# Kernel tuning notes

Hardware: AMD Instinct MI355X
Metric: run time of the kernel (lower is better)

Reference implementation:

```python
import jax, jax.numpy as jnp
import numpy as np

B, CIN, COUT, K, LDIM, HW = 16, 512, 512, 3, 512, 32


def setup_inputs() -> dict:
    key = jax.random.key(0)
    ks = jax.random.split(key, 4)
    return {
        "x": jax.random.normal(ks[0], (B, CIN, HW, HW), jnp.float32),
        "w": jax.random.normal(ks[1], (B, LDIM), jnp.float32),
        "mod_w": jax.random.normal(ks[2], (CIN, LDIM), jnp.float32) * 0.02,
        "mod_b": jnp.zeros((CIN,), jnp.float32),
        "ln_g": jnp.ones((CIN,), jnp.float32),
        "ln_b": jnp.zeros((CIN,), jnp.float32),
        "weight": jax.random.normal(ks[3], (COUT, CIN, K, K), jnp.float32) * 0.02,
        "scale": jnp.ones((1, CIN, 1, 1), jnp.float32),
    }


def reference(x, w, mod_w, mod_b, ln_g, ln_b, weight, scale):
    eps = 1e-8
    b, cin, H, W = x.shape
    cout, _, k, _ = weight.shape
    # modulation MLP: Linear -> LayerNorm -> LeakyReLU(0.2)
    s = w @ mod_w.T + mod_b                                   # [b, cin]
    mu = s.mean(-1, keepdims=True)
    var = s.var(-1, keepdims=True)
    s = (s - mu) * jax.lax.rsqrt(var + 1e-5) * ln_g + ln_b
    s = jnp.where(s >= 0, s, 0.2 * s)
    # modulate per-sample weights: [b, cout, cin, k, k]
    s = s.reshape(b, 1, cin, 1, 1) * scale.reshape(1, 1, cin, 1, 1)
    wmod = weight[None] * s
    # demodulate
    d = jax.lax.rsqrt(jnp.sum(wmod * wmod, axis=(2, 3, 4)) + eps)  # [b, cout]
    wmod = wmod * d.reshape(b, cout, 1, 1, 1)
    # batch-as-groups conv2d
    wg = wmod.reshape(b * cout, cin, k, k)
    xg = x.reshape(1, b * cin, H, W)
    pad = k // 2
    out = jax.lax.conv_general_dilated(
        xg, wg, window_strides=(1, 1), padding=[(pad, pad), (pad, pad)],
        dimension_numbers=("NCHW", "OIHW", "NCHW"), feature_group_count=b)
    return out.reshape(b, cout, H, W)
```

## Files before the change

### kernel.cpp

```cpp
#include <hip/hip_runtime.h>

typedef unsigned short u16;
typedef __bf16 bf16x8 __attribute__((ext_vector_type(8)));
typedef float  f32x16 __attribute__((ext_vector_type(16)));

__device__ __forceinline__ u16 f2bf(float f) {
    union { float f; unsigned u; } v; v.f = f;
    return (u16)((v.u + 0x7fffu + ((v.u >> 16) & 1u)) >> 16);
}

#define GLD16(gsrc, ldst) \
    __builtin_amdgcn_global_load_lds( \
        (const __attribute__((address_space(1))) void*)(gsrc), \
        (__attribute__((address_space(3))) void*)(ldst), 16, 0, 0)

__global__ __launch_bounds__(256) void lin_kernel(
    const float* __restrict__ w, const float* __restrict__ mod_w,
    const float* __restrict__ mod_b, float* __restrict__ s_raw)
{
    int gw = (blockIdx.x * 256 + threadIdx.x) >> 6;
    int lane = threadIdx.x & 63;
    int b = gw >> 9, c = gw & 511;
    const float* wr = w + b * 512;
    const float* mr = mod_w + (size_t)c * 512;
    float a = 0.f;
#pragma unroll
    for (int i = 0; i < 8; ++i)
        a = fmaf(wr[lane + i * 64], mr[lane + i * 64], a);
    for (int off = 32; off; off >>= 1) a += __shfl_down(a, off);
    if (!lane) s_raw[gw] = a + mod_b[c];
}

__global__ __launch_bounds__(512) void norm_kernel(
    const float* __restrict__ s_raw, const float* __restrict__ ln_g,
    const float* __restrict__ ln_b, const float* __restrict__ scale,
    float* __restrict__ s_eff)
{
    int b = blockIdx.x, c = threadIdx.x;
    __shared__ float rs[512], rq[512];
    float s = s_raw[b * 512 + c];
    rs[c] = s; rq[c] = s * s;
    __syncthreads();
    for (int off = 256; off; off >>= 1) {
        if (c < off) { rs[c] += rs[c + off]; rq[c] += rq[c + off]; }
        __syncthreads();
    }
    float mean = rs[0] * (1.f / 512.f);
    float var  = rq[0] * (1.f / 512.f) - mean * mean;
    float sn = (s - mean) * rsqrtf(var + 1e-5f) * ln_g[c] + ln_b[c];
    sn = sn >= 0.f ? sn : 0.2f * sn;
    s_eff[b * 512 + c] = sn * scale[c];
}

__global__ __launch_bounds__(256) void wsq_kernel(
    const float* __restrict__ weight, float* __restrict__ wsq, u16* __restrict__ wbfT)
{
    int idx = blockIdx.x * 256 + threadIdx.x;
    int co = idx >> 9, ci = idx & 511;
    int cg = ci >> 3, cj = ci & 7;
    const float* wp = weight + (size_t)idx * 9;
    float s = 0.f;
#pragma unroll
    for (int p = 0; p < 9; ++p) {
        float v = wp[p];
        s += v * v;
        wbfT[((size_t)(p * 64 + cg) * 512 + co) * 8 + cj] = f2bf(v);
    }
    wsq[idx] = s;
}

__global__ __launch_bounds__(256) void xs_kernel(
    const float* __restrict__ x, const float* __restrict__ s_eff,
    u16* __restrict__ xs)
{
    const int bh = blockIdx.x;
    const int b = bh >> 5, h = bh & 31;
    __shared__ float tile[64][33];
    for (int c0 = 0; c0 < 512; c0 += 64) {
        if (c0) __syncthreads();
        for (int idx = threadIdx.x; idx < 2048; idx += 256) {
            int c = idx >> 5, ww = idx & 31;
            tile[c][ww] = x[(((size_t)b * 512 + c0 + c) * 32 + h) * 32 + ww]
                          * s_eff[b * 512 + c0 + c];
        }
        __syncthreads();
        for (int idx = threadIdx.x; idx < 2048; idx += 256) {
            int ww = idx >> 6, c = idx & 63;
            xs[((b * 32 + h) * 32 + ww) * 512 + c0 + c] = f2bf(tile[c][ww]);
        }
    }
}

__global__ __launch_bounds__(256) void dsc_kernel(
    const float* __restrict__ s_eff, const float* __restrict__ wsq,
    float* __restrict__ dsc)
{
    int gw = (blockIdx.x * 256 + threadIdx.x) >> 6;
    int lane = threadIdx.x & 63;
    int b = gw >> 9, co = gw & 511;
    float a = 0.f;
#pragma unroll
    for (int i = 0; i < 8; ++i) {
        int cin = lane + i * 64;
        float se = s_eff[b * 512 + cin];
        a += se * se * wsq[co * 512 + cin];
    }
    for (int off = 32; off; off >>= 1) a += __shfl_down(a, off);
    if (!lane) dsc[gw] = rsqrtf(a + 1e-8f);
}

__global__ void zfill_kernel(float* p) { p[threadIdx.x] = 0.f; }

__global__ __launch_bounds__(512) void conv_kernel(
    const u16* __restrict__ wbfT,
    const u16* __restrict__ xs,
    const float* __restrict__ dsc,
    const u16* __restrict__ zp,
    float* __restrict__ out)
{
    __shared__ __align__(16) u16 ldsA[2][24576];
    __shared__ __align__(16) u16 ldsB[2][8192];

    const int tid  = threadIdx.x;
    const int lane = tid & 63;
    const int wv   = tid >> 6;
    const int wm   = wv >> 1;
    const int wn   = wv & 1;
    const int l31  = lane & 31;
    const int kc8  = lane >> 5;

    const int bx = blockIdx.x;
    const int mt = bx & 1;
    const int nt = bx >> 1;
    const int b  = nt >> 3;
    const int h0 = (nt & 7) << 2;

    const u16* xsb = xs + (size_t)b * (32 * 32 * 512);

    const u16* asrc[6];
#pragma unroll
    for (int k = 0; k < 6; ++k) {
        int ch = tid + k * 512;
        int pp = ch >> 10, kc = (ch >> 8) & 3, co = ch & 255;
        asrc[k] = wbfT + ((size_t)(pp * 64 + kc) * 512 + mt * 256 + co) * 8;
    }
    auto stageA = [&](int buf) {
        char* d = (char*)ldsA[buf] + wv * 1024;
#pragma unroll
        for (int k = 0; k < 6; ++k) GLD16(asrc[k], d + k * 8192);
    };
    auto advA = [&](int dkf) {
#pragma unroll
        for (int k = 0; k < 6; ++k) asrc[k] += (long)dkf * 4096;
    };

    const u16* bsrc[2]; bool binb[2];
#pragma unroll
    for (int k = 0; k < 2; ++k) {
        int ch = tid + k * 512;
        int kc = ch / 204, p = ch % 204;
        int rr = p / 34, cc = p % 34;
        int hh = h0 - 1 + rr, ww = cc - 1;
        binb[k] = (ch < 816) && ((unsigned)hh < 32u) && ((unsigned)ww < 32u);
        bsrc[k] = xsb + (hh * 32 + ww) * 512 + kc * 8;
    }
    auto stageB = [&](int buf) {
        char* d = (char*)ldsB[buf] + wv * 1024;
        GLD16(binb[0] ? bsrc[0] : zp, d);
        GLD16(binb[1] ? bsrc[1] : zp, d + 8192);
    };

    f32x16 acc[2][2] = {};

    stageA(0);
    advA(192);
    stageB(0);
    __syncthreads();

    int pidx = 0;
    for (int r = 0; r < 16; ++r) {
        const char* Bb = (const char*)ldsB[r & 1];
        const bool lastR = (r == 15);

#pragma unroll
        for (int phi = 0; phi < 3; ++phi) {
            const int abuf = pidx & 1;
            const char* Ab = (const char*)ldsA[abuf];
            const bool lastPhase = lastR && (phi == 2);

            if (!lastPhase) {
                stageA(abuf ^ 1);
                advA(phi == 1 ? -380 : 192);
            }
            if (phi == 1 && !lastR) {
#pragma unroll
                for (int k = 0; k < 2; ++k) bsrc[k] += 32;
                stageB((r + 1) & 1);
            }

            bf16x8 af[3][2][2], bfr[3][2][2];
#pragma unroll
            for (int pp = 0; pp < 3; ++pp)
#pragma unroll
                for (int kk = 0; kk < 2; ++kk) {
                    const int kc = kk * 2 + kc8;
#pragma unroll
                    for (int mf = 0; mf < 2; ++mf) {
                        int co = wm * 64 + mf * 32 + l31;
                        af[pp][mf][kk] = *reinterpret_cast<const bf16x8*>(
                            Ab + (((pp * 4 + kc) * 256 + co) << 4));
                    }
#pragma unroll
                    for (int nf = 0; nf < 2; ++nf) {
                        int p = (wn * 2 + nf + phi) * 34 + l31 + pp;
                        bfr[pp][nf][kk] = *reinterpret_cast<const bf16x8*>(
                            Bb + ((kc * 204 + p) << 4));
                    }
                }

#pragma unroll
            for (int pp = 0; pp < 3; ++pp)
#pragma unroll
                for (int kk = 0; kk < 2; ++kk) {
                    acc[0][0] = __builtin_amdgcn_mfma_f32_32x32x16_bf16(
                        af[pp][0][kk], bfr[pp][0][kk], acc[0][0], 0, 0, 0);
                    acc[0][1] = __builtin_amdgcn_mfma_f32_32x32x16_bf16(
                        af[pp][0][kk], bfr[pp][1][kk], acc[0][1], 0, 0, 0);
                    acc[1][0] = __builtin_amdgcn_mfma_f32_32x32x16_bf16(
                        af[pp][1][kk], bfr[pp][0][kk], acc[1][0], 0, 0, 0);
                    acc[1][1] = __builtin_amdgcn_mfma_f32_32x32x16_bf16(
                        af[pp][1][kk], bfr[pp][1][kk], acc[1][1], 0, 0, 0);
                }

            if (!lastPhase) __syncthreads();
            ++pidx;
        }
    }

    const float* db = dsc + b * 512;
#pragma unroll
    for (int mf = 0; mf < 2; ++mf) {
#pragma unroll
        for (int nf = 0; nf < 2; ++nf) {
            const int h = h0 + wn * 2 + nf, w = l31;
#pragma unroll
            for (int q = 0; q < 16; ++q) {
                int row = (q & 3) + 8 * (q >> 2) + 4 * kc8;
                int co  = mt * 256 + wm * 64 + mf * 32 + row;
                out[(((size_t)b * 512 + co) * 32 + h) * 32 + w]
                    = acc[mf][nf][q] * db[co];
            }
        }
    }
}

extern "C" void kernel_launch(void* const* d_in, const int* in_sizes, int n_in,
                              void* d_out, int out_size, void* d_ws, size_t ws_size,
                              hipStream_t stream) {
    const float* x      = (const float*)d_in[0];
    const float* w      = (const float*)d_in[1];
    const float* mod_w  = (const float*)d_in[2];
    const float* mod_b  = (const float*)d_in[3];
    const float* ln_g   = (const float*)d_in[4];
    const float* ln_b   = (const float*)d_in[5];
    const float* weight = (const float*)d_in[6];
    const float* scale  = (const float*)d_in[7];
    float* out = (float*)d_out;

    char* ws = (char*)d_ws;
    float* s_raw = (float*)(ws);
    float* dsc   = (float*)(ws);
    float* s_eff = (float*)(ws + 32768);
    float* wsq   = (float*)(ws + 65536);
    u16*   wbfT  = (u16*)(ws + 65536 + 1048576);
    u16*   xs    = (u16*)(ws + 65536 + 1048576 + 4718592);
    if (ws_size < 22609920u) return;

    lin_kernel <<<2048, 256, 0, stream>>>(w, mod_w, mod_b, s_raw);
    wsq_kernel <<<1024, 256, 0, stream>>>(weight, wsq, wbfT);
    norm_kernel<<<16, 512, 0, stream>>>(s_raw, ln_g, ln_b, scale, s_eff);
    xs_kernel  <<<512, 256, 0, stream>>>(x, s_eff, xs);
    dsc_kernel <<<2048, 256, 0, stream>>>(s_eff, wsq, dsc);
    zfill_kernel<<<1, 1024, 0, stream>>>(s_eff);
    conv_kernel<<<256, 512, 0, stream>>>(wbfT, xs, dsc, (const u16*)s_eff, out);
}
```

Before: 121.4 us.

## Load weight fragments directly from global into registers, drop LDS A staging

The conv kernel no longer stages the modulated weight tiles through shared memory. Each wave reads its A fragments straight from global memory into registers, double-buffered one phase ahead. The input tile is now staged through registers and ordinary LDS stores, and only one barrier per row iteration remains instead of one per phase. This removes the large A LDS buffer and most barriers, but adds register pressure and duplicate global reads of weights across waves that share the same rows.

```diff
diff --git a/kernel.cpp b/kernel.cpp
--- a/kernel.cpp
+++ b/kernel.cpp
@@ -8,11 +8,6 @@
     union { float f; unsigned u; } v; v.f = f;
     return (u16)((v.u + 0x7fffu + ((v.u >> 16) & 1u)) >> 16);
 }
-
-#define GLD16(gsrc, ldst) \
-    __builtin_amdgcn_global_load_lds( \
-        (const __attribute__((address_space(1))) void*)(gsrc), \
-        (__attribute__((address_space(3))) void*)(ldst), 16, 0, 0)
 
 __global__ __launch_bounds__(256) void lin_kernel(
     const float* __restrict__ w, const float* __restrict__ mod_w,
@@ -118,7 +113,6 @@
     const u16* __restrict__ zp,
     float* __restrict__ out)
 {
-    __shared__ __align__(16) u16 ldsA[2][24576];
     __shared__ __align__(16) u16 ldsB[2][8192];
 
     const int tid  = threadIdx.x;
@@ -137,24 +131,10 @@
 
     const u16* xsb = xs + (size_t)b * (32 * 32 * 512);
 
-    const u16* asrc[6];
-#pragma unroll
-    for (int k = 0; k < 6; ++k) {
-        int ch = tid + k * 512;
-        int pp = ch >> 10, kc = (ch >> 8) & 3, co = ch & 255;
-        asrc[k] = wbfT + ((size_t)(pp * 64 + kc) * 512 + mt * 256 + co) * 8;
-    }
-    auto stageA = [&](int buf) {
-        char* d = (char*)ldsA[buf] + wv * 1024;
-#pragma unroll
-        for (int k = 0; k < 6; ++k) GLD16(asrc[k], d + k * 8192);
-    };
-    auto advA = [&](int dkf) {
-#pragma unroll
-        for (int k = 0; k < 6; ++k) asrc[k] += (long)dkf * 4096;
-    };
-
-    const u16* bsrc[2]; bool binb[2];
+    const u16* abase = wbfT + ((size_t)(mt * 256 + wm * 64 + l31)) * 8
+                            + (size_t)kc8 * 4096;
+
+    const u16* bptr[2]; bool binb[2]; int bdst[2];
 #pragma unroll
     for (int k = 0; k < 2; ++k) {
         int ch = tid + k * 512;
@@ -162,78 +142,89 @@
         int rr = p / 34, cc = p % 34;
         int hh = h0 - 1 + rr, ww = cc - 1;
         binb[k] = (ch < 816) && ((unsigned)hh < 32u) && ((unsigned)ww < 32u);
-        bsrc[k] = xsb + (hh * 32 + ww) * 512 + kc * 8;
-    }
-    auto stageB = [&](int buf) {
-        char* d = (char*)ldsB[buf] + wv * 1024;
-        GLD16(binb[0] ? bsrc[0] : zp, d);
-        GLD16(binb[1] ? bsrc[1] : zp, d + 8192);
-    };
+        bptr[k] = binb[k] ? xsb + (hh * 32 + ww) * 512 + kc * 8 : zp;
+        bdst[k] = ch * 16;
+    }
+    const int badv[2] = { binb[0] ? 32 : 0, binb[1] ? 32 : 0 };
 
     f32x16 acc[2][2] = {};
-
-    stageA(0);
-    advA(192);
-    stageB(0);
-    __syncthreads();
-
-    int pidx = 0;
+    bf16x8 af[2][3][2][2];
+    uint4  bst[2];
+
+#pragma unroll
+    for (int k = 0; k < 2; ++k) {
+        bst[k] = *reinterpret_cast<const uint4*>(bptr[k]);
+        bptr[k] += badv[k];
+        *reinterpret_cast<uint4*>((char*)ldsB[0] + bdst[k]) = bst[k];
+    }
+#pragma unroll
+    for (int pp = 0; pp < 3; ++pp)
+#pragma unroll
+        for (int mf = 0; mf < 2; ++mf)
+#pragma unroll
+            for (int kk = 0; kk < 2; ++kk)
+                af[0][pp][mf][kk] = *reinterpret_cast<const bf16x8*>(
+                    abase + (size_t)(pp * 64 + 2 * kk) * 4096 + mf * 256);
+    asm volatile("s_waitcnt lgkmcnt(0)" ::: "memory");
+    __builtin_amdgcn_s_barrier();
+
+#pragma unroll
     for (int r = 0; r < 16; ++r) {
-        const char* Bb = (const char*)ldsB[r & 1];
-        const bool lastR = (r == 15);
-
 #pragma unroll
         for (int phi = 0; phi < 3; ++phi) {
-            const int abuf = pidx & 1;
-            const char* Ab = (const char*)ldsA[abuf];
-            const bool lastPhase = lastR && (phi == 2);
-
-            if (!lastPhase) {
-                stageA(abuf ^ 1);
-                advA(phi == 1 ? -380 : 192);
-            }
-            if (phi == 1 && !lastR) {
-#pragma unroll
-                for (int k = 0; k < 2; ++k) bsrc[k] += 32;
-                stageB((r + 1) & 1);
-            }
-
-            bf16x8 af[3][2][2], bfr[3][2][2];
+            const int t = r * 3 + phi;
+            const char* Bb = (const char*)ldsB[r & 1];
+
+            if (t + 1 < 48) {
+                const int rn = (t + 1) / 3, pn = (t + 1) % 3;
+#pragma unroll
+                for (int pp = 0; pp < 3; ++pp)
+#pragma unroll
+                    for (int mf = 0; mf < 2; ++mf)
+#pragma unroll
+                        for (int kk = 0; kk < 2; ++kk)
+                            af[(t + 1) & 1][pp][mf][kk] =
+                                *reinterpret_cast<const bf16x8*>(
+                                    abase + (size_t)((pn * 3 + pp) * 64
+                                        + 4 * rn + 2 * kk) * 4096 + mf * 256);
+            }
+
+            if (phi == 0 && r < 15) {
+#pragma unroll
+                for (int k = 0; k < 2; ++k) {
+                    bst[k] = *reinterpret_cast<const uint4*>(bptr[k]);
+                    bptr[k] += badv[k];
+                }
+            }
+
 #pragma unroll
             for (int pp = 0; pp < 3; ++pp)
 #pragma unroll
                 for (int kk = 0; kk < 2; ++kk) {
                     const int kc = kk * 2 + kc8;
-#pragma unroll
-                    for (int mf = 0; mf < 2; ++mf) {
-                        int co = wm * 64 + mf * 32 + l31;
-                        af[pp][mf][kk] = *reinterpret_cast<const bf16x8*>(
-                            Ab + (((pp * 4 + kc) * 256 + co) << 4));
-                    }
-#pragma unroll
-                    for (int nf = 0; nf < 2; ++nf) {
-                        int p = (wn * 2 + nf + phi) * 34 + l31 + pp;
-                        bfr[pp][nf][kk] = *reinterpret_cast<const bf16x8*>(
-                            Bb + ((kc * 204 + p) << 4));
-                    }
+                    const int p0 = (wn * 2 + phi) * 34 + l31 + pp;
+                    bf16x8 b0 = *reinterpret_cast<const bf16x8*>(
+                        Bb + ((kc * 204 + p0) << 4));
+                    bf16x8 b1 = *reinterpret_cast<const bf16x8*>(
+                        Bb + ((kc * 204 + p0 + 34) << 4));
+                    acc[0][0] = __builtin_amdgcn_mfma_f32_32x32x16_bf16(
+                        af[t & 1][pp][0][kk], b0, acc[0][0], 0, 0, 0);
+                    acc[0][1] = __builtin_amdgcn_mfma_f32_32x32x16_bf16(
+                        af[t & 1][pp][0][kk], b1, acc[0][1], 0, 0, 0);
+                    acc[1][0] = __builtin_amdgcn_mfma_f32_32x32x16_bf16(
+                        af[t & 1][pp][1][kk], b0, acc[1][0], 0, 0, 0);
+                    acc[1][1] = __builtin_amdgcn_mfma_f32_32x32x16_bf16(
+                        af[t & 1][pp][1][kk], b1, acc[1][1], 0, 0, 0);
                 }
 
-#pragma unroll
-            for (int pp = 0; pp < 3; ++pp)
-#pragma unroll
-                for (int kk = 0; kk < 2; ++kk) {
-                    acc[0][0] = __builtin_amdgcn_mfma_f32_32x32x16_bf16(
-                        af[pp][0][kk], bfr[pp][0][kk], acc[0][0], 0, 0, 0);
-                    acc[0][1] = __builtin_amdgcn_mfma_f32_32x32x16_bf16(
-                        af[pp][0][kk], bfr[pp][1][kk], acc[0][1], 0, 0, 0);
-                    acc[1][0] = __builtin_amdgcn_mfma_f32_32x32x16_bf16(
-                        af[pp][1][kk], bfr[pp][0][kk], acc[1][0], 0, 0, 0);
-                    acc[1][1] = __builtin_amdgcn_mfma_f32_32x32x16_bf16(
-                        af[pp][1][kk], bfr[pp][1][kk], acc[1][1], 0, 0, 0);
-                }
-
-            if (!lastPhase) __syncthreads();
-            ++pidx;
+            if (phi == 2 && r < 15) {
+                char* d = (char*)ldsB[(r + 1) & 1];
+#pragma unroll
+                for (int k = 0; k < 2; ++k)
+                    *reinterpret_cast<uint4*>(d + bdst[k]) = bst[k];
+                asm volatile("s_waitcnt lgkmcnt(0)" ::: "memory");
+                __builtin_amdgcn_s_barrier();
+            }
         }
     }
 
```

Result: slower. 195.3 us (+60.9%).

## Halve conv block to 256 threads with 128x64 warp tiles per wave

Applied to the files above, without the earlier changes.

The conv kernel moves from 512 to 256 threads per block, with launch bounds set to one block. Each wave now computes four M fragments instead of two, so it reuses every B fragment across more MFMAs, and each thread issues twice as many global-to-LDS loads. The pipeline barrier becomes an explicit vmcnt(0) wait plus s_barrier, and LDS fragment loads are issued per pp step rather than all at once. In exchange, each wave holds more accumulator registers and the CU has fewer waves to hide latency with, given only 256 blocks.

```diff
diff --git a/kernel.cpp b/kernel.cpp
--- a/kernel.cpp
+++ b/kernel.cpp
@@ -111,7 +111,7 @@
 
 __global__ void zfill_kernel(float* p) { p[threadIdx.x] = 0.f; }
 
-__global__ __launch_bounds__(512) void conv_kernel(
+__global__ __launch_bounds__(256, 1) void conv_kernel(
     const u16* __restrict__ wbfT,
     const u16* __restrict__ xs,
     const float* __restrict__ dsc,
@@ -137,45 +137,35 @@
 
     const u16* xsb = xs + (size_t)b * (32 * 32 * 512);
 
-    const u16* asrc[6];
-#pragma unroll
-    for (int k = 0; k < 6; ++k) {
-        int ch = tid + k * 512;
-        int pp = ch >> 10, kc = (ch >> 8) & 3, co = ch & 255;
-        asrc[k] = wbfT + ((size_t)(pp * 64 + kc) * 512 + mt * 256 + co) * 8;
-    }
-    auto stageA = [&](int buf) {
-        char* d = (char*)ldsA[buf] + wv * 1024;
-#pragma unroll
-        for (int k = 0; k < 6; ++k) GLD16(asrc[k], d + k * 8192);
-    };
-    auto advA = [&](int dkf) {
-#pragma unroll
-        for (int k = 0; k < 6; ++k) asrc[k] += (long)dkf * 4096;
-    };
-
-    const u16* bsrc[2]; bool binb[2];
-#pragma unroll
-    for (int k = 0; k < 2; ++k) {
-        int ch = tid + k * 512;
+    const u16* A0 = wbfT + ((size_t)(mt * 256 + tid)) * 8;
+    char* adst = (char*)nullptr;
+
+    const u16* bsrc[4];
+#pragma unroll
+    for (int k = 0; k < 4; ++k) {
+        int ch = tid + k * 256;
         int kc = ch / 204, p = ch % 204;
         int rr = p / 34, cc = p % 34;
         int hh = h0 - 1 + rr, ww = cc - 1;
-        binb[k] = (ch < 816) && ((unsigned)hh < 32u) && ((unsigned)ww < 32u);
-        bsrc[k] = xsb + (hh * 32 + ww) * 512 + kc * 8;
-    }
-    auto stageB = [&](int buf) {
-        char* d = (char*)ldsB[buf] + wv * 1024;
-        GLD16(binb[0] ? bsrc[0] : zp, d);
-        GLD16(binb[1] ? bsrc[1] : zp, d + 8192);
-    };
-
-    f32x16 acc[2][2] = {};
-
-    stageA(0);
-    advA(192);
-    stageB(0);
-    __syncthreads();
+        bool inb = (ch < 816) && ((unsigned)hh < 32u) && ((unsigned)ww < 32u);
+        bsrc[k] = inb ? xsb + (hh * 32 + ww) * 512 + kc * 8 : zp;
+    }
+
+    f32x16 acc[4][2] = {};
+
+    {
+        char* d = (char*)ldsA[0] + wv * 1024;
+#pragma unroll
+        for (int k = 0; k < 12; ++k)
+            GLD16(A0 + (size_t)((k >> 2) * 64 + (k & 3)) * 4096, d + k * 4096);
+        A0 += (size_t)192 * 4096;
+        char* db = (char*)ldsB[0] + wv * 1024;
+#pragma unroll
+        for (int k = 0; k < 3; ++k) GLD16(bsrc[k], db + k * 4096);
+        if (tid < 48) GLD16(bsrc[3], db + 3 * 4096);
+    }
+    asm volatile("s_waitcnt vmcnt(0)" ::: "memory");
+    __builtin_amdgcn_s_barrier();
 
     int pidx = 0;
     for (int r = 0; r < 16; ++r) {
@@ -189,64 +179,70 @@
             const bool lastPhase = lastR && (phi == 2);
 
             if (!lastPhase) {
-                stageA(abuf ^ 1);
-                advA(phi == 1 ? -380 : 192);
+                char* d = (char*)ldsA[abuf ^ 1] + wv * 1024;
+#pragma unroll
+                for (int k = 0; k < 12; ++k)
+                    GLD16(A0 + (size_t)((k >> 2) * 64 + (k & 3)) * 4096,
+                          d + k * 4096);
+                A0 += (size_t)(phi == 1 ? -380 : 192) * 4096;
             }
             if (phi == 1 && !lastR) {
 #pragma unroll
-                for (int k = 0; k < 2; ++k) bsrc[k] += 32;
-                stageB((r + 1) & 1);
-            }
-
-            bf16x8 af[3][2][2], bfr[3][2][2];
-#pragma unroll
-            for (int pp = 0; pp < 3; ++pp)
+                for (int k = 0; k < 4; ++k) bsrc[k] += 32;
+                char* db = (char*)ldsB[(r + 1) & 1] + wv * 1024;
+#pragma unroll
+                for (int k = 0; k < 3; ++k) GLD16(bsrc[k], db + k * 4096);
+                if (tid < 48) GLD16(bsrc[3], db + 3 * 4096);
+            }
+
+#pragma unroll
+            for (int pp = 0; pp < 3; ++pp) {
+                bf16x8 af[4][2], bfr[2][2];
 #pragma unroll
                 for (int kk = 0; kk < 2; ++kk) {
                     const int kc = kk * 2 + kc8;
 #pragma unroll
-                    for (int mf = 0; mf < 2; ++mf) {
-                        int co = wm * 64 + mf * 32 + l31;
-                        af[pp][mf][kk] = *reinterpret_cast<const bf16x8*>(
-                            Ab + (((pp * 4 + kc) * 256 + co) << 4));
+                    for (int mf = 0; mf < 4; ++mf) {
+                        const int cl = wm * 128 + mf * 32 + l31;
+                        af[mf][kk] = *reinterpret_cast<const bf16x8*>(
+                            Ab + (pp * 4 + kc) * 4096 + cl * 16);
                     }
 #pragma unroll
                     for (int nf = 0; nf < 2; ++nf) {
-                        int p = (wn * 2 + nf + phi) * 34 + l31 + pp;
-                        bfr[pp][nf][kk] = *reinterpret_cast<const bf16x8*>(
+                        const int p = (wn * 2 + nf + phi) * 34 + l31 + pp;
+                        bfr[nf][kk] = *reinterpret_cast<const bf16x8*>(
                             Bb + ((kc * 204 + p) << 4));
                     }
                 }
-
-#pragma unroll
-            for (int pp = 0; pp < 3; ++pp)
-#pragma unroll
-                for (int kk = 0; kk < 2; ++kk) {
-                    acc[0][0] = __builtin_amdgcn_mfma_f32_32x32x16_bf16(
-                        af[pp][0][kk], bfr[pp][0][kk], acc[0][0], 0, 0, 0);
-                    acc[0][1] = __builtin_amdgcn_mfma_f32_32x32x16_bf16(
-                        af[pp][0][kk], bfr[pp][1][kk], acc[0][1], 0, 0, 0);
-                    acc[1][0] = __builtin_amdgcn_mfma_f32_32x32x16_bf16(
-                        af[pp][1][kk], bfr[pp][0][kk], acc[1][0], 0, 0, 0);
-                    acc[1][1] = __builtin_amdgcn_mfma_f32_32x32x16_bf16(
-                        af[pp][1][kk], bfr[pp][1][kk], acc[1][1], 0, 0, 0);
-                }
-
-            if (!lastPhase) __syncthreads();
+#pragma unroll
+                for (int kk = 0; kk < 2; ++kk)
+#pragma unroll
+                    for (int mf = 0; mf < 4; ++mf) {
+                        acc[mf][0] = __builtin_amdgcn_mfma_f32_32x32x16_bf16(
+                            af[mf][kk], bfr[0][kk], acc[mf][0], 0, 0, 0);
+                        acc[mf][1] = __builtin_amdgcn_mfma_f32_32x32x16_bf16(
+                            af[mf][kk], bfr[1][kk], acc[mf][1], 0, 0, 0);
+                    }
+            }
+
+            if (!lastPhase) {
+                asm volatile("s_waitcnt vmcnt(0)" ::: "memory");
+                __builtin_amdgcn_s_barrier();
+            }
             ++pidx;
         }
     }
 
     const float* db = dsc + b * 512;
 #pragma unroll
-    for (int mf = 0; mf < 2; ++mf) {
+    for (int mf = 0; mf < 4; ++mf) {
 #pragma unroll
         for (int nf = 0; nf < 2; ++nf) {
             const int h = h0 + wn * 2 + nf, w = l31;
 #pragma unroll
             for (int q = 0; q < 16; ++q) {
                 int row = (q & 3) + 8 * (q >> 2) + 4 * kc8;
-                int co  = mt * 256 + wm * 64 + mf * 32 + row;
+                int co  = mt * 256 + wm * 128 + mf * 32 + row;
                 out[(((size_t)b * 512 + co) * 32 + h) * 32 + w]
                     = acc[mf][nf][q] * db[co];
             }
@@ -282,5 +278,5 @@
     xs_kernel  <<<512, 256, 0, stream>>>(x, s_eff, xs);
     dsc_kernel <<<2048, 256, 0, stream>>>(s_eff, wsq, dsc);
     zfill_kernel<<<1, 1024, 0, stream>>>(s_eff);
-    conv_kernel<<<256, 512, 0, stream>>>(wbfT, xs, dsc, (const u16*)s_eff, out);
-}
+    conv_kernel<<<256, 256, 0, stream>>>(wbfT, xs, dsc, (const u16*)s_eff, out);
+}
```

After: 127.8 us. 5.3% more time.
